# Kernel optimization log

Measured on AMD Instinct MI355X. Metric: run time of the kernel, lower is better.

Reference implementation:

```python
import jax, jax.numpy as jnp
import numpy as np

LMBDA = 100.0
GAMMA = 0.5


def _get_mask(evals1, evals2, gamma):
    # evals1, evals2: [B, K]; returns D: [B, K, K]
    scale = jnp.maximum(jnp.max(evals1, axis=1), jnp.max(evals2, axis=1))[:, None]
    e1 = evals1 / scale
    e2 = evals2 / scale
    g1 = (e1 ** gamma)[:, None, :]   # [B, 1, K]
    g2 = (e2 ** gamma)[:, :, None]   # [B, K, 1]
    M_re = g2 / (g2 ** 2 + 1) - g1 / (g1 ** 2 + 1)
    M_im = 1.0 / (g2 ** 2 + 1) - 1.0 / (g1 ** 2 + 1)
    return M_re ** 2 + M_im ** 2


def setup_inputs() -> dict:
    key = jax.random.key(0)
    ks = jax.random.split(key, 6)
    B, Vx, Vy, C, K = 8, 20000, 20000, 256, 128
    return {
        "feat_x": jax.random.normal(ks[0], (B, Vx, C), dtype=jnp.float32),
        "feat_y": jax.random.normal(ks[1], (B, Vy, C), dtype=jnp.float32),
        "evals_x": jax.random.uniform(ks[2], (B, K), dtype=jnp.float32, minval=0.01, maxval=1.0),
        "evals_y": jax.random.uniform(ks[3], (B, K), dtype=jnp.float32, minval=0.01, maxval=1.0),
        "evecs_trans_x": jax.random.normal(ks[4], (B, K, Vx), dtype=jnp.float32),
        "evecs_trans_y": jax.random.normal(ks[5], (B, K, Vy), dtype=jnp.float32),
    }


def reference(feat_x, feat_y, evals_x, evals_y, evecs_trans_x, evecs_trans_y):
    # Spectral projections of features
    A = jnp.einsum('bkv,bvc->bkc', evecs_trans_x, feat_x)   # [B, K, C]
    Bm = jnp.einsum('bkv,bvc->bkc', evecs_trans_y, feat_y)  # [B, K, C]
    D = _get_mask(evals_x, evals_y, GAMMA)                  # [B, K, K]
    AAt = jnp.einsum('bkc,bjc->bkj', A, A)                  # [B, K, K]
    BAt = jnp.einsum('bkc,bjc->bkj', Bm, A)                 # [B, K, K]
    # Batched over (B, i): solve (AAt + lmbda*diag(D[b,i])) x = BAt[b,i]
    Dmats = jax.vmap(jax.vmap(jnp.diag))(D)                 # [B, K, K, K]
    M = AAt[:, None, :, :] + LMBDA * Dmats                  # [B, K, K, K]
    Cxy = jnp.linalg.solve(M, BAt[..., None])[..., 0]       # rows: Cxy[b, i, :]
    return Cxy
```

## Files before the change

kernel.cpp:

```cpp
#include <hip/hip_runtime.h>
#include <hip/hip_bf16.h>

namespace {

constexpr int NB = 8;
constexpr int NV = 20000;
constexpr int NC = 256;
constexpr int NK = 128;
constexpr float LMBDA = 100.0f;
constexpr int KSTEP = 32;
constexpr int CHUNKS = 16;

typedef __attribute__((ext_vector_type(8))) short bf16x8;
typedef __attribute__((ext_vector_type(4))) float f32x4;

__device__ __forceinline__ uint cvtpk(float a, float c) {
  uint r;
  asm("v_cvt_pk_bf16_f32 %0, %1, %2" : "=v"(r) : "v"(a), "v"(c));
  return r;
}

template <int MODE>
__global__ __launch_bounds__(512, 4) void proj_mfma(
    const float* __restrict__ Ex, const float* __restrict__ Fx,
    const float* __restrict__ Ey, const float* __restrict__ Fy,
    float* __restrict__ A, float* __restrict__ Bm, float* __restrict__ P)
{
  extern __shared__ ushort smem[];

  const int chunk = blockIdx.x;
  const int ct    = blockIdx.y;
  const int bs    = blockIdx.z;
  const int b     = bs >> 1;
  const int side  = bs & 1;
  const float* __restrict__ E = (side ? Ey : Ex) + (size_t)b * NK * NV;
  const float* __restrict__ F = (side ? Fy : Fx) + (size_t)b * NV * NC;
  float* __restrict__ Out = (side ? Bm : A) + (size_t)b * NK * NC;
  const int cb = ct * 128;

  const int start = chunk * 39 + (chunk > 0 ? 1 : 0);
  const int nsteps = 39 + (chunk == 0 ? 1 : 0);
  const int v0 = start * KSTEP;

  const int tid  = threadIdx.x;
  const int lane = tid & 63;
  const int w    = tid >> 6;
  const int wm   = w >> 2;
  const int wn   = w & 3;
  const int lrow = lane >> 4;
  const int lcol = lane & 15;

  const int ek  = tid >> 2;
  const int evg = tid & 3;
  const int ef  = ek >> 4;
  const int entE = (((ek & 15) + evg * 4) & 15) + evg * 16;
  const float* Erow = E + (size_t)ek * NV + v0 + evg * 8;

  const int fp  = tid & 15;
  const int fc0 = (tid >> 4) * 4;
  const int fcg = fc0 >> 4;
  const int fclow = fc0 & 15;
  const int fvg = fp >> 2;
  const int fsp = fp & 3;

  f32x4 acc[4][2];
#pragma unroll
  for (int fi = 0; fi < 4; fi++)
#pragma unroll
    for (int ni = 0; ni < 2; ni++) acc[fi][ni] = (f32x4)0.f;

  const int entA = (((lcol) + lrow * 4) & 15) + lrow * 16;

  auto loadE = [&](int t, float4& a0, float4& a1) {
    const float* p = Erow + t * KSTEP;
    a0 = *(const float4*)(p);
    a1 = *(const float4*)(p + 4);
  };
  auto loadF = [&](int t, float4& b0, float4& b1) {
    const float* p = F + (size_t)(v0 + t * KSTEP + 2 * fp) * NC + cb + fc0;
    b0 = *(const float4*)(p);
    b1 = *(const float4*)(p + NC);
  };

  auto stage = [&](int buf, float4 e0, float4 e1, float4 f0, float4 f1) {
    ushort* AHb = smem + buf * 16384;
    ushort* BHb = AHb + 8192;
    const float v[8] = {e0.x, e0.y, e0.z, e0.w, e1.x, e1.y, e1.z, e1.w};
    uint hiw[4], low[4];
#pragma unroll
    for (int i = 0; i < 4; i++) {
      float a = v[2 * i], c = v[2 * i + 1];
      uint h = cvtpk(a, c);
      low[i] = cvtpk(a - __uint_as_float(h << 16),
                     c - __uint_as_float(h & 0xffff0000u));
      hiw[i] = h;
    }
    *(uint4*)(AHb + ef * 512 + entE * 8)        = make_uint4(hiw[0], hiw[1], hiw[2], hiw[3]);
    *(uint4*)(AHb + 4096 + ef * 512 + entE * 8) = make_uint4(low[0], low[1], low[2], low[3]);

    const float* fa = (const float*)&f0;
    const float* fb = (const float*)&f1;
#pragma unroll
    for (int j = 0; j < 4; j++) {
      int ent = ((fclow + j + fcg) & 15) + fvg * 16;
      float a = fa[j], c = fb[j];
      uint h = cvtpk(a, c);
      uint l = cvtpk(a - __uint_as_float(h << 16),
                     c - __uint_as_float(h & 0xffff0000u));
      *(uint*)(BHb + fcg * 512 + ent * 8 + 2 * fsp) = h;
      *(uint*)(BHb + 4096 + fcg * 512 + ent * 8 + 2 * fsp) = l;
    }
  };

  auto domfma = [&](int buf) {
    const ushort* AHb = smem + buf * 16384;
    const ushort* BHb = AHb + 8192;
    bf16x8 bHf[2], bLf[2];
#pragma unroll
    for (int ni = 0; ni < 2; ni++) {
      int cg = wn * 2 + ni;
      int entB = ((lcol + cg) & 15) + lrow * 16;
      bHf[ni] = *(const bf16x8*)(BHb + cg * 512 + entB * 8);
      bLf[ni] = *(const bf16x8*)(BHb + 4096 + cg * 512 + entB * 8);
    }
#pragma unroll
    for (int fi = 0; fi < 4; fi++) {
      bf16x8 aH = *(const bf16x8*)(AHb + (wm * 4 + fi) * 512 + entA * 8);
      bf16x8 aL = *(const bf16x8*)(AHb + 4096 + (wm * 4 + fi) * 512 + entA * 8);
#pragma unroll
      for (int ni = 0; ni < 2; ni++) {
        acc[fi][ni] = __builtin_amdgcn_mfma_f32_16x16x32_bf16(aH, bHf[ni], acc[fi][ni], 0, 0, 0);
        acc[fi][ni] = __builtin_amdgcn_mfma_f32_16x16x32_bf16(aH, bLf[ni], acc[fi][ni], 0, 0, 0);
        acc[fi][ni] = __builtin_amdgcn_mfma_f32_16x16x32_bf16(aL, bHf[ni], acc[fi][ni], 0, 0, 0);
      }
    }
  };

  float4 eA0, eA1, fA0, fA1, eB0, eB1, fB0, fB1;
  loadE(0, eA0, eA1); loadF(0, fA0, fA1);
  stage(0, eA0, eA1, fA0, fA1);
  {
    const int t1 = (1 < nsteps) ? 1 : 0;
    loadE(t1, eB0, eB1); loadF(t1, fB0, fB1);
  }
  __syncthreads();

  for (int s = 0; s < nsteps; s++) {
    const int bufc = s & 1;
    if (s + 1 < nsteps) {
      if ((s & 1) == 0) stage(bufc ^ 1, eB0, eB1, fB0, fB1);
      else              stage(bufc ^ 1, eA0, eA1, fA0, fA1);
    }
    if (s + 2 < nsteps) {
      if ((s & 1) == 0) { loadE(s + 2, eA0, eA1); loadF(s + 2, fA0, fA1); }
      else              { loadE(s + 2, eB0, eB1); loadF(s + 2, fB0, fB1); }
    }
    domfma(bufc);
    __syncthreads();
  }

#pragma unroll
  for (int fi = 0; fi < 4; fi++) {
#pragma unroll
    for (int ni = 0; ni < 2; ni++) {
      const float* av = (const float*)&acc[fi][ni];
#pragma unroll
      for (int q = 0; q < 4; q++) {
        int row = wm * 64 + fi * 16 + lrow * 4 + q;
        int col = cb + wn * 32 + ni * 16 + lcol;
        if (MODE == 0) {
          P[(((size_t)chunk * 16 + bs) * NK + row) * NC + col] = av[q];
        } else {
          atomicAdd(&Out[(size_t)row * NC + col], av[q]);
        }
      }
    }
  }
}

__global__ __launch_bounds__(256) void reduce_kernel(
    const float* __restrict__ P, float* __restrict__ AB)
{
  const int g = blockIdx.x * 256 + threadIdx.x;
  const int bsi = g >> 13;
  const int rem4 = g & 8191;
  const int side = bsi & 1, b = bsi >> 1;
  float4 s = make_float4(0.f, 0.f, 0.f, 0.f);
#pragma unroll
  for (int ch = 0; ch < CHUNKS; ch++) {
    float4 v = *(const float4*)(P + (((size_t)ch * 16 + bsi) * 8192 + rem4) * 4);
    s.x += v.x; s.y += v.y; s.z += v.z; s.w += v.w;
  }
  *(float4*)(AB + ((size_t)side * 262144 + (size_t)b * 8192 * 4 + (size_t)rem4 * 4)) = s;
}

__global__ __launch_bounds__(256) void gram_kernel(
    const float* __restrict__ A, const float* __restrict__ Bm,
    float* __restrict__ AAt, float* __restrict__ BAt)
{
  const int i0 = blockIdx.x * 8;
  const int b  = blockIdx.y;
  __shared__ float Xi[16][260];
  const float* __restrict__ Ab = A  + (size_t)b * NK * NC;
  const float* __restrict__ Bb = Bm + (size_t)b * NK * NC;
  const int tid = threadIdx.x;
  for (int idx = tid; idx < 16 * 64; idx += 256) {
    int row = idx >> 6, c4 = idx & 63;
    const float* src = (row < 8) ? (Ab + (size_t)(i0 + row) * NC)
                                 : (Bb + (size_t)(i0 + row - 8) * NC);
    *(float4*)&Xi[row][c4 * 4] = *(const float4*)(src + c4 * 4);
  }
  __syncthreads();
  const int j = tid & 127;
  const int m = tid >> 7;
  const float* __restrict__ Arow = Ab + (size_t)j * NC;
  float accv[8];
#pragma unroll
  for (int i = 0; i < 8; i++) accv[i] = 0.f;
  for (int c4 = 0; c4 < 64; c4++) {
    float4 a4 = *(const float4*)(Arow + c4 * 4);
#pragma unroll
    for (int i = 0; i < 8; i++) {
      float4 x4 = *(const float4*)&Xi[m * 8 + i][c4 * 4];
      accv[i] = fmaf(x4.x, a4.x, accv[i]);
      accv[i] = fmaf(x4.y, a4.y, accv[i]);
      accv[i] = fmaf(x4.z, a4.z, accv[i]);
      accv[i] = fmaf(x4.w, a4.w, accv[i]);
    }
  }
  float* Outp = (m ? BAt : AAt) + ((size_t)b * NK + i0) * NK + j;
#pragma unroll
  for (int i = 0; i < 8; i++) Outp[(size_t)i * NK] = accv[i];
}

__global__ __launch_bounds__(256) void mask_kernel(
    const float* __restrict__ evx, const float* __restrict__ evy,
    float* __restrict__ Dm)
{
  const int b = blockIdx.x;
  const int tid = threadIdx.x;
  __shared__ float red[256];
  __shared__ float t1x[128], t2x[128], t1y[128], t2y[128];
  float v = (tid < 128) ? evx[b * 128 + tid] : evy[b * 128 + (tid - 128)];
  red[tid] = v;
  __syncthreads();
  for (int sft = 128; sft > 0; sft >>= 1) {
    if (tid < sft) red[tid] = fmaxf(red[tid], red[tid + sft]);
    __syncthreads();
  }
  const float inv_scale = 1.0f / red[0];
  if (tid < 128) {
    float e = evx[b * 128 + tid] * inv_scale;
    float g = sqrtf(e);
    float d = 1.f / (g * g + 1.f);
    t1x[tid] = g * d;  t2x[tid] = d;
  } else {
    int i = tid - 128;
    float e = evy[b * 128 + i] * inv_scale;
    float g = sqrtf(e);
    float d = 1.f / (g * g + 1.f);
    t1y[i] = g * d;  t2y[i] = d;
  }
  __syncthreads();
  float* __restrict__ Db = Dm + (size_t)b * NK * NK;
  for (int idx = tid; idx < NK * NK; idx += 256) {
    int i = idx >> 7, jj = idx & 127;
    float re = t1y[i] - t1x[jj];
    float im = t2y[i] - t2x[jj];
    Db[idx] = re * re + im * im;
  }
}

__global__ __launch_bounds__(512) void invert_kernel(
    const float* __restrict__ AAt, float* __restrict__ Sinv)
{
  extern __shared__ float sh[];
  float* M = sh;
  float* R = sh + 128 * 132;
  const int b = blockIdx.x;
  const int tid = threadIdx.x;
  const float* __restrict__ Sb = AAt + (size_t)b * NK * NK;
  for (int idx = tid; idx < NK * NK; idx += 512) {
    M[(idx >> 7) * 132 + (idx & 127)] = Sb[idx];
  }
  __syncthreads();
  const int r = tid & 127;
  const int h = tid >> 7;
  const int c0 = h * 32;

  for (int p = 0; p < 16; p++) {
    const int J0 = p * 8;
    const bool inJ = (r >= J0) && (r < J0 + 8);
    const int i0 = r - J0;

    float g[8][8];
#pragma unroll
    for (int i = 0; i < 8; i++)
#pragma unroll
      for (int j = 0; j < 8; j++) g[i][j] = M[(J0 + i) * 132 + J0 + j];

#pragma unroll
    for (int j = 0; j < 8; j++) {
      const float invd = 1.f / g[j][j];
#pragma unroll
      for (int i = 0; i < 8; i++) {
        if (i == j) continue;
        const float f = g[i][j] * invd;
#pragma unroll
        for (int c = 0; c < 8; c++) {
          if (c == j) continue;
          g[i][c] = fmaf(-f, g[j][c], g[i][c]);
        }
        g[i][j] = -f;
      }
#pragma unroll
      for (int c = 0; c < 8; c++) {
        if (c == j) continue;
        g[j][c] *= invd;
      }
      g[j][j] = invd;
    }

    float c8[8];
    if (inJ) {
#pragma unroll
      for (int q = 0; q < 8; q++) {
        float v = 0.f;
#pragma unroll
        for (int i = 0; i < 8; i++)
          if (i0 == i) v = g[i][q];
        c8[q] = ((i0 == q) ? 1.f : 0.f) - v;
      }
    } else {
      float mr8[8];
#pragma unroll
      for (int k = 0; k < 8; k++) mr8[k] = M[r * 132 + J0 + k];
#pragma unroll
      for (int q = 0; q < 8; q++) {
        float a = 0.f;
#pragma unroll
        for (int k = 0; k < 8; k++) a = fmaf(mr8[k], g[k][q], a);
        c8[q] = a;
      }
    }

    if (inJ) {
#pragma unroll
      for (int i = 0; i < 8; i++)
        *(float4*)&R[i0 * 132 + c0 + i * 4] = *(const float4*)&M[r * 132 + c0 + i * 4];
    }
    __syncthreads();

    float4 m[8];
#pragma unroll
    for (int i = 0; i < 8; i++) m[i] = *(const float4*)&M[r * 132 + c0 + i * 4];
#pragma unroll
    for (int k = 0; k < 8; k++) {
      const float f = c8[k];
#pragma unroll
      for (int i = 0; i < 8; i++) {
        float4 rv = *(const float4*)&R[k * 132 + c0 + i * 4];
        m[i].x = fmaf(-f, rv.x, m[i].x);
        m[i].y = fmaf(-f, rv.y, m[i].y);
        m[i].z = fmaf(-f, rv.z, m[i].z);
        m[i].w = fmaf(-f, rv.w, m[i].w);
      }
    }
    {
      const bool panelH = (h == (J0 >> 5));
      const int q4 = (J0 & 31) >> 2;
      float sp[8];
#pragma unroll
      for (int q = 0; q < 8; q++)
        sp[q] = -c8[q] + ((inJ && i0 == q) ? 1.f : 0.f);
      const float4 lo = make_float4(sp[0], sp[1], sp[2], sp[3]);
      const float4 hi = make_float4(sp[4], sp[5], sp[6], sp[7]);
#pragma unroll
      for (int i = 0; i < 8; i++) {
        if (panelH && i == q4)     m[i] = lo;
        if (panelH && i == q4 + 1) m[i] = hi;
      }
    }
#pragma unroll
    for (int i = 0; i < 8; i++) *(float4*)&M[r * 132 + c0 + i * 4] = m[i];
    __syncthreads();
  }

  float* __restrict__ Ob = Sinv + (size_t)b * NK * NK;
  for (int idx = tid; idx < NK * NK; idx += 512) {
    Ob[idx] = M[(idx >> 7) * 132 + (idx & 127)];
  }
}

__global__ __launch_bounds__(256) void ns_kernel(
    const float* __restrict__ AAt, const float* __restrict__ Xin,
    float* __restrict__ Xout)
{
  extern __shared__ float sh[];
  float* S_ = sh;
  float* X_ = sh + 128 * 132;
  float* W_ = X_ + 128 * 133;
  const int tile = blockIdx.x;
  const int b    = blockIdx.y;
  const int j0   = tile * 32;
  const int tid  = threadIdx.x;
  const float* __restrict__ Sg = AAt + (size_t)b * NK * NK;
  const float* __restrict__ Xg = Xin + (size_t)b * NK * NK;
  float* __restrict__ Og       = Xout + (size_t)b * NK * NK;
  for (int idx = tid; idx < NK * NK; idx += 256) {
    int rr = idx >> 7, cc = idx & 127;
    S_[rr * 132 + cc] = Sg[idx];
    X_[rr * 133 + cc] = Xg[idx];
  }
  __syncthreads();

  const int kg  = tid >> 4;
  const int jj2 = (tid & 15) * 2;

  float aw[8][2];
#pragma unroll
  for (int u = 0; u < 8; u++) { aw[u][0] = 0.f; aw[u][1] = 0.f; }
  for (int m = 0; m < NK; m++) {
    const float x0 = X_[m * 133 + j0 + jj2];
    const float x1 = X_[m * 133 + j0 + jj2 + 1];
    float4 s0 = *(const float4*)&S_[m * 132 + kg * 8];
    float4 s1 = *(const float4*)&S_[m * 132 + kg * 8 + 4];
    const float sv[8] = {s0.x, s0.y, s0.z, s0.w, s1.x, s1.y, s1.z, s1.w};
#pragma unroll
    for (int u = 0; u < 8; u++) {
      aw[u][0] = fmaf(sv[u], x0, aw[u][0]);
      aw[u][1] = fmaf(sv[u], x1, aw[u][1]);
    }
  }
#pragma unroll
  for (int u = 0; u < 8; u++) {
#pragma unroll
    for (int j = 0; j < 2; j++) {
      const int k = kg * 8 + u;
      float val = -aw[u][j];
      if (k == j0 + jj2 + j) val += 2.f;
      W_[k * 33 + jj2 + j] = val;
    }
  }
  __syncthreads();

  float ax[8][2];
#pragma unroll
  for (int u = 0; u < 8; u++) { ax[u][0] = 0.f; ax[u][1] = 0.f; }
  for (int k = 0; k < NK; k++) {
    const float w0 = W_[k * 33 + jj2];
    const float w1 = W_[k * 33 + jj2 + 1];
#pragma unroll
    for (int u = 0; u < 8; u++) {
      const float x = X_[(kg * 8 + u) * 133 + k];
      ax[u][0] = fmaf(x, w0, ax[u][0]);
      ax[u][1] = fmaf(x, w1, ax[u][1]);
    }
  }
#pragma unroll
  for (int u = 0; u < 8; u++) {
    Og[(size_t)(kg * 8 + u) * NK + j0 + jj2]     = ax[u][0];
    Og[(size_t)(kg * 8 + u) * NK + j0 + jj2 + 1] = ax[u][1];
  }
}

__global__ __launch_bounds__(256) void solve_kernel(
    const float* __restrict__ Sinv, const float* __restrict__ BAt,
    const float* __restrict__ Dm, float* __restrict__ Cxy)
{
  extern __shared__ float sh[];
  float* SinvS = sh;
  float* ZS    = sh + 128 * 132;
  const int tile = blockIdx.x;
  const int b    = blockIdx.y;
  const int i0b  = tile * 32;
  const int tid  = threadIdx.x;
  const float* __restrict__ Sb = Sinv + (size_t)b * NK * NK;
  const float* __restrict__ Rb = BAt  + (size_t)b * NK * NK;
  const float* __restrict__ Db = Dm   + (size_t)b * NK * NK;
  for (int idx = tid; idx < NK * NK; idx += 256) {
    SinvS[(idx >> 7) * 132 + (idx & 127)] = Sb[idx];
  }
  for (int idx = tid; idx < 32 * NK; idx += 256) {
    int rr = idx >> 7, cc = idx & 127;
    ZS[rr * 133 + cc] = Rb[(size_t)(i0b + rr) * NK + cc];
  }
  __syncthreads();

  const int il = (tid >> 4) * 2;
  const int r0 = (tid & 15) * 8;
  float Y[2][8], X[2][8];
#pragma unroll
  for (int u = 0; u < 2; u++)
#pragma unroll
    for (int v = 0; v < 8; v++) Y[u][v] = 0.f;

  for (int c = 0; c < NK; c++) {
    float4 s0 = *(const float4*)&SinvS[c * 132 + r0];
    float4 s1 = *(const float4*)&SinvS[c * 132 + r0 + 4];
#pragma unroll
    for (int u = 0; u < 2; u++) {
      float z = ZS[(il + u) * 133 + c];
      Y[u][0] = fmaf(z, s0.x, Y[u][0]);
      Y[u][1] = fmaf(z, s0.y, Y[u][1]);
      Y[u][2] = fmaf(z, s0.z, Y[u][2]);
      Y[u][3] = fmaf(z, s0.w, Y[u][3]);
      Y[u][4] = fmaf(z, s1.x, Y[u][4]);
      Y[u][5] = fmaf(z, s1.y, Y[u][5]);
      Y[u][6] = fmaf(z, s1.z, Y[u][6]);
      Y[u][7] = fmaf(z, s1.w, Y[u][7]);
    }
  }
#pragma unroll
  for (int u = 0; u < 2; u++)
#pragma unroll
    for (int v = 0; v < 8; v++) X[u][v] = Y[u][v];

  for (int it = 0; it < 2; it++) {
    __syncthreads();
#pragma unroll
    for (int u = 0; u < 2; u++) {
      const float* drow = Db + (size_t)(i0b + il + u) * NK + r0;
      float* zrow = ZS + (il + u) * 133 + r0;
#pragma unroll
      for (int v = 0; v < 8; v++) zrow[v] = LMBDA * drow[v] * X[u][v];
    }
    __syncthreads();
#pragma unroll
    for (int u = 0; u < 2; u++)
#pragma unroll
      for (int v = 0; v < 8; v++) X[u][v] = Y[u][v];
    for (int c = 0; c < NK; c++) {
      float4 s0 = *(const float4*)&SinvS[c * 132 + r0];
      float4 s1 = *(const float4*)&SinvS[c * 132 + r0 + 4];
#pragma unroll
      for (int u = 0; u < 2; u++) {
        float z = ZS[(il + u) * 133 + c];
        X[u][0] = fmaf(-z, s0.x, X[u][0]);
        X[u][1] = fmaf(-z, s0.y, X[u][1]);
        X[u][2] = fmaf(-z, s0.z, X[u][2]);
        X[u][3] = fmaf(-z, s0.w, X[u][3]);
        X[u][4] = fmaf(-z, s1.x, X[u][4]);
        X[u][5] = fmaf(-z, s1.y, X[u][5]);
        X[u][6] = fmaf(-z, s1.z, X[u][6]);
        X[u][7] = fmaf(-z, s1.w, X[u][7]);
      }
    }
  }
  float* __restrict__ Ob = Cxy + ((size_t)b * NK + i0b + il) * NK + r0;
#pragma unroll
  for (int u = 0; u < 2; u++) {
    float4 o0 = make_float4(X[u][0], X[u][1], X[u][2], X[u][3]);
    float4 o1 = make_float4(X[u][4], X[u][5], X[u][6], X[u][7]);
    *(float4*)(Ob + (size_t)u * NK)     = o0;
    *(float4*)(Ob + (size_t)u * NK + 4) = o1;
  }
}

}

extern "C" void kernel_launch(void* const* d_in, const int* in_sizes, int n_in,
                              void* d_out, int out_size, void* d_ws, size_t ws_size,
                              hipStream_t stream) {
  (void)in_sizes; (void)n_in; (void)out_size;
  const float* feat_x  = (const float*)d_in[0];
  const float* feat_y  = (const float*)d_in[1];
  const float* evals_x = (const float*)d_in[2];
  const float* evals_y = (const float*)d_in[3];
  const float* etx     = (const float*)d_in[4];
  const float* ety     = (const float*)d_in[5];
  float* out = (float*)d_out;
  float* ws  = (float*)d_ws;

  float* A    = ws;
  float* Bm   = ws + 262144;
  float* AAt  = ws + 524288;
  float* BAt  = ws + 655360;
  float* Dm   = ws + 786432;
  float* Sinv = ws + 917504;
  float* P    = ws + 1048576;
  float* Sinv2 = Bm;

  const bool use_partial = ws_size >= (size_t)(1048576 + 8388608) * 4;

  constexpr int PROJ_LDS  = 2 * 16384 * 2;
  constexpr int INV_LDS   = (128 * 132 + 8 * 132) * 4;
  constexpr int NS_LDS    = (128 * 132 + 128 * 133 + 128 * 33) * 4;
  constexpr int SOLVE_LDS = (128 * 132 + 32 * 133) * 4;
  hipFuncSetAttribute((const void*)proj_mfma<0>,
                      hipFuncAttributeMaxDynamicSharedMemorySize, PROJ_LDS);
  hipFuncSetAttribute((const void*)proj_mfma<1>,
                      hipFuncAttributeMaxDynamicSharedMemorySize, PROJ_LDS);
  hipFuncSetAttribute((const void*)invert_kernel,
                      hipFuncAttributeMaxDynamicSharedMemorySize, INV_LDS);
  hipFuncSetAttribute((const void*)ns_kernel,
                      hipFuncAttributeMaxDynamicSharedMemorySize, NS_LDS);
  hipFuncSetAttribute((const void*)solve_kernel,
                      hipFuncAttributeMaxDynamicSharedMemorySize, SOLVE_LDS);

  if (use_partial) {
    proj_mfma<0><<<dim3(CHUNKS, 2, 16), 512, PROJ_LDS, stream>>>(etx, feat_x, ety, feat_y, A, Bm, P);
    reduce_kernel<<<dim3(512), 256, 0, stream>>>(P, ws);
  } else {
    hipMemsetAsync(A, 0, (size_t)524288 * sizeof(float), stream);
    proj_mfma<1><<<dim3(CHUNKS, 2, 16), 512, PROJ_LDS, stream>>>(etx, feat_x, ety, feat_y, A, Bm, P);
  }
  gram_kernel<<<dim3(16, 8), 256, 0, stream>>>(A, Bm, AAt, BAt);
  mask_kernel<<<dim3(8), 256, 0, stream>>>(evals_x, evals_y, Dm);
  invert_kernel<<<dim3(8), 512, INV_LDS, stream>>>(AAt, Sinv);
  ns_kernel<<<dim3(4, 8), 256, NS_LDS, stream>>>(AAt, Sinv, Sinv2);
  ns_kernel<<<dim3(4, 8), 256, NS_LDS, stream>>>(AAt, Sinv2, Sinv);
  solve_kernel<<<dim3(4, 8), 256, SOLVE_LDS, stream>>>(Sinv, BAt, Dm, out);
}
```

Before: 267.1 us.

## Halve projection block to 256 threads with larger per-wave MFMA tiles

Reworks the projection GEMM kernel from 512 to 256 threads per block, so each wave now computes a 64x64 output tile (4x4 MFMA fragments) instead of 64x32. The global-load and LDS staging mapping is rewritten: each thread loads 16 contiguous evec floats and eight float2 feature rows, then packs them into the hi/lo bf16 split tiles. The goal is more B-fragment reuse per LDS read and fewer threads sharing the same staging work. In exchange each thread holds more accumulators and load registers, which cuts occupancy and leaves fewer waves to hide memory latency.

```diff
diff --git a/kernel.cpp b/kernel.cpp
--- a/kernel.cpp
+++ b/kernel.cpp
@@ -21,7 +21,7 @@
 }
 
 template <int MODE>
-__global__ __launch_bounds__(512, 4) void proj_mfma(
+__global__ __launch_bounds__(256, 2) void proj_mfma(
     const float* __restrict__ Ex, const float* __restrict__ Fx,
     const float* __restrict__ Ey, const float* __restrict__ Fy,
     float* __restrict__ A, float* __restrict__ Bm, float* __restrict__ P)
@@ -45,80 +45,99 @@
   const int tid  = threadIdx.x;
   const int lane = tid & 63;
   const int w    = tid >> 6;
-  const int wm   = w >> 2;
-  const int wn   = w & 3;
+  const int wm   = w >> 1;
+  const int wn   = w & 1;
   const int lrow = lane >> 4;
   const int lcol = lane & 15;
 
-  const int ek  = tid >> 2;
-  const int evg = tid & 3;
-  const int ef  = ek >> 4;
-  const int entE = (((ek & 15) + evg * 4) & 15) + evg * 16;
-  const float* Erow = E + (size_t)ek * NV + v0 + evg * 8;
-
-  const int fp  = tid & 15;
-  const int fc0 = (tid >> 4) * 4;
-  const int fcg = fc0 >> 4;
-  const int fclow = fc0 & 15;
-  const int fvg = fp >> 2;
-  const int fsp = fp & 3;
-
-  f32x4 acc[4][2];
+  const int erow = tid >> 1;
+  const int eh   = tid & 1;
+  const float* Erow = E + (size_t)erow * NV + v0 + eh * 16;
+
+  const int bg  = tid >> 6;
+  const int c0  = (tid & 63) * 2;
+  const int c1  = c0 + 1;
+  const float* Fbase = F + (size_t)(v0 + bg * 8) * NC + cb + c0;
+
+  f32x4 acc[4][4];
 #pragma unroll
   for (int fi = 0; fi < 4; fi++)
 #pragma unroll
-    for (int ni = 0; ni < 2; ni++) acc[fi][ni] = (f32x4)0.f;
+    for (int ni = 0; ni < 4; ni++) acc[fi][ni] = (f32x4)0.f;
 
   const int entA = (((lcol) + lrow * 4) & 15) + lrow * 16;
 
-  auto loadE = [&](int t, float4& a0, float4& a1) {
+  auto loadE = [&](int t, float4* e) {
     const float* p = Erow + t * KSTEP;
-    a0 = *(const float4*)(p);
-    a1 = *(const float4*)(p + 4);
+    e[0] = *(const float4*)(p);
+    e[1] = *(const float4*)(p + 4);
+    e[2] = *(const float4*)(p + 8);
+    e[3] = *(const float4*)(p + 12);
   };
-  auto loadF = [&](int t, float4& b0, float4& b1) {
-    const float* p = F + (size_t)(v0 + t * KSTEP + 2 * fp) * NC + cb + fc0;
-    b0 = *(const float4*)(p);
-    b1 = *(const float4*)(p + NC);
+  auto loadF = [&](int t, float2* f) {
+    const float* p = Fbase + (size_t)t * KSTEP * NC;
+#pragma unroll
+    for (int j = 0; j < 8; j++) f[j] = *(const float2*)(p + (size_t)j * NC);
   };
 
-  auto stage = [&](int buf, float4 e0, float4 e1, float4 f0, float4 f1) {
+  auto stage = [&](int buf, const float4* e, const float2* f) {
     ushort* AHb = smem + buf * 16384;
     ushort* BHb = AHb + 8192;
-    const float v[8] = {e0.x, e0.y, e0.z, e0.w, e1.x, e1.y, e1.z, e1.w};
-    uint hiw[4], low[4];
-#pragma unroll
-    for (int i = 0; i < 4; i++) {
-      float a = v[2 * i], c = v[2 * i + 1];
-      uint h = cvtpk(a, c);
-      low[i] = cvtpk(a - __uint_as_float(h << 16),
-                     c - __uint_as_float(h & 0xffff0000u));
-      hiw[i] = h;
-    }
-    *(uint4*)(AHb + ef * 512 + entE * 8)        = make_uint4(hiw[0], hiw[1], hiw[2], hiw[3]);
-    *(uint4*)(AHb + 4096 + ef * 512 + entE * 8) = make_uint4(low[0], low[1], low[2], low[3]);
-
-    const float* fa = (const float*)&f0;
-    const float* fb = (const float*)&f1;
-#pragma unroll
-    for (int j = 0; j < 4; j++) {
-      int ent = ((fclow + j + fcg) & 15) + fvg * 16;
-      float a = fa[j], c = fb[j];
-      uint h = cvtpk(a, c);
-      uint l = cvtpk(a - __uint_as_float(h << 16),
-                     c - __uint_as_float(h & 0xffff0000u));
-      *(uint*)(BHb + fcg * 512 + ent * 8 + 2 * fsp) = h;
-      *(uint*)(BHb + 4096 + fcg * 512 + ent * 8 + 2 * fsp) = l;
+    {
+      const int frag = erow >> 4;
+      const int r15  = erow & 15;
+#pragma unroll
+      for (int i = 0; i < 2; i++) {
+        const int vg  = 2 * eh + i;
+        const int ent = ((r15 + vg * 4) & 15) + vg * 16;
+        const float4 x = e[2 * i];
+        const float4 y = e[2 * i + 1];
+        uint h0 = cvtpk(x.x, x.y), h1 = cvtpk(x.z, x.w);
+        uint h2 = cvtpk(y.x, y.y), h3 = cvtpk(y.z, y.w);
+        uint l0 = cvtpk(x.x - __uint_as_float(h0 << 16),
+                        x.y - __uint_as_float(h0 & 0xffff0000u));
+        uint l1 = cvtpk(x.z - __uint_as_float(h1 << 16),
+                        x.w - __uint_as_float(h1 & 0xffff0000u));
+        uint l2 = cvtpk(y.x - __uint_as_float(h2 << 16),
+                        y.y - __uint_as_float(h2 & 0xffff0000u));
+        uint l3 = cvtpk(y.z - __uint_as_float(h3 << 16),
+                        y.w - __uint_as_float(h3 & 0xffff0000u));
+        *(uint4*)(AHb + frag * 512 + ent * 8)        = make_uint4(h0, h1, h2, h3);
+        *(uint4*)(AHb + 4096 + frag * 512 + ent * 8) = make_uint4(l0, l1, l2, l3);
+      }
+    }
+    {
+      const int frag = c0 >> 4;
+      const int ent0 = (((c0 & 15) + frag) & 15) + bg * 16;
+      const int ent1 = (((c1 & 15) + frag) & 15) + bg * 16;
+      uint h0[4], l0[4], h1[4], l1[4];
+#pragma unroll
+      for (int i = 0; i < 4; i++) {
+        const float a0 = f[2 * i].x, b0 = f[2 * i + 1].x;
+        const float a1 = f[2 * i].y, b1 = f[2 * i + 1].y;
+        uint h = cvtpk(a0, b0);
+        h0[i] = h;
+        l0[i] = cvtpk(a0 - __uint_as_float(h << 16),
+                      b0 - __uint_as_float(h & 0xffff0000u));
+        h = cvtpk(a1, b1);
+        h1[i] = h;
+        l1[i] = cvtpk(a1 - __uint_as_float(h << 16),
+                      b1 - __uint_as_float(h & 0xffff0000u));
+      }
+      *(uint4*)(BHb + frag * 512 + ent0 * 8)        = make_uint4(h0[0], h0[1], h0[2], h0[3]);
+      *(uint4*)(BHb + 4096 + frag * 512 + ent0 * 8) = make_uint4(l0[0], l0[1], l0[2], l0[3]);
+      *(uint4*)(BHb + frag * 512 + ent1 * 8)        = make_uint4(h1[0], h1[1], h1[2], h1[3]);
+      *(uint4*)(BHb + 4096 + frag * 512 + ent1 * 8) = make_uint4(l1[0], l1[1], l1[2], l1[3]);
     }
   };
 
   auto domfma = [&](int buf) {
     const ushort* AHb = smem + buf * 16384;
     const ushort* BHb = AHb + 8192;
-    bf16x8 bHf[2], bLf[2];
-#pragma unroll
-    for (int ni = 0; ni < 2; ni++) {
-      int cg = wn * 2 + ni;
+    bf16x8 bHf[4], bLf[4];
+#pragma unroll
+    for (int ni = 0; ni < 4; ni++) {
+      int cg = wn * 4 + ni;
       int entB = ((lcol + cg) & 15) + lrow * 16;
       bHf[ni] = *(const bf16x8*)(BHb + cg * 512 + entB * 8);
       bLf[ni] = *(const bf16x8*)(BHb + 4096 + cg * 512 + entB * 8);
@@ -128,7 +147,7 @@
       bf16x8 aH = *(const bf16x8*)(AHb + (wm * 4 + fi) * 512 + entA * 8);
       bf16x8 aL = *(const bf16x8*)(AHb + 4096 + (wm * 4 + fi) * 512 + entA * 8);
 #pragma unroll
-      for (int ni = 0; ni < 2; ni++) {
+      for (int ni = 0; ni < 4; ni++) {
         acc[fi][ni] = __builtin_amdgcn_mfma_f32_16x16x32_bf16(aH, bHf[ni], acc[fi][ni], 0, 0, 0);
         acc[fi][ni] = __builtin_amdgcn_mfma_f32_16x16x32_bf16(aH, bLf[ni], acc[fi][ni], 0, 0, 0);
         acc[fi][ni] = __builtin_amdgcn_mfma_f32_16x16x32_bf16(aL, bHf[ni], acc[fi][ni], 0, 0, 0);
@@ -136,24 +155,25 @@
     }
   };
 
-  float4 eA0, eA1, fA0, fA1, eB0, eB1, fB0, fB1;
-  loadE(0, eA0, eA1); loadF(0, fA0, fA1);
-  stage(0, eA0, eA1, fA0, fA1);
+  float4 eA[4]; float2 fA[8];
+  float4 eB[4]; float2 fB[8];
+  loadE(0, eA); loadF(0, fA);
+  stage(0, eA, fA);
   {
     const int t1 = (1 < nsteps) ? 1 : 0;
-    loadE(t1, eB0, eB1); loadF(t1, fB0, fB1);
+    loadE(t1, eB); loadF(t1, fB);
   }
   __syncthreads();
 
   for (int s = 0; s < nsteps; s++) {
     const int bufc = s & 1;
     if (s + 1 < nsteps) {
-      if ((s & 1) == 0) stage(bufc ^ 1, eB0, eB1, fB0, fB1);
-      else              stage(bufc ^ 1, eA0, eA1, fA0, fA1);
+      if ((s & 1) == 0) stage(bufc ^ 1, eB, fB);
+      else              stage(bufc ^ 1, eA, fA);
     }
     if (s + 2 < nsteps) {
-      if ((s & 1) == 0) { loadE(s + 2, eA0, eA1); loadF(s + 2, fA0, fA1); }
-      else              { loadE(s + 2, eB0, eB1); loadF(s + 2, fB0, fB1); }
+      if ((s & 1) == 0) { loadE(s + 2, eA); loadF(s + 2, fA); }
+      else              { loadE(s + 2, eB); loadF(s + 2, fB); }
     }
     domfma(bufc);
     __syncthreads();
@@ -162,12 +182,12 @@
 #pragma unroll
   for (int fi = 0; fi < 4; fi++) {
 #pragma unroll
-    for (int ni = 0; ni < 2; ni++) {
+    for (int ni = 0; ni < 4; ni++) {
       const float* av = (const float*)&acc[fi][ni];
 #pragma unroll
       for (int q = 0; q < 4; q++) {
         int row = wm * 64 + fi * 16 + lrow * 4 + q;
-        int col = cb + wn * 32 + ni * 16 + lcol;
+        int col = cb + wn * 64 + ni * 16 + lcol;
         if (MODE == 0) {
           P[(((size_t)chunk * 16 + bs) * NK + row) * NC + col] = av[q];
         } else {
@@ -599,11 +619,11 @@
                       hipFuncAttributeMaxDynamicSharedMemorySize, SOLVE_LDS);
 
   if (use_partial) {
-    proj_mfma<0><<<dim3(CHUNKS, 2, 16), 512, PROJ_LDS, stream>>>(etx, feat_x, ety, feat_y, A, Bm, P);
+    proj_mfma<0><<<dim3(CHUNKS, 2, 16), 256, PROJ_LDS, stream>>>(etx, feat_x, ety, feat_y, A, Bm, P);
     reduce_kernel<<<dim3(512), 256, 0, stream>>>(P, ws);
   } else {
     hipMemsetAsync(A, 0, (size_t)524288 * sizeof(float), stream);
-    proj_mfma<1><<<dim3(CHUNKS, 2, 16), 512, PROJ_LDS, stream>>>(etx, feat_x, ety, feat_y, A, Bm, P);
+    proj_mfma<1><<<dim3(CHUNKS, 2, 16), 256, PROJ_LDS, stream>>>(etx, feat_x, ety, feat_y, A, Bm, P);
   }
   gram_kernel<<<dim3(16, 8), 256, 0, stream>>>(A, Bm, AAt, BAt);
   mask_kernel<<<dim3(8), 256, 0, stream>>>(evals_x, evals_y, Dm);
```

Measured after the change: 272.3 us. About the same (+2.0%).

## Double chunk count, single-buffer static LDS, atomically fold chunk pairs

Applied to the files above, without the earlier changes.

Splits the vertex dimension into 32 chunks instead of 16, so twice as many blocks run the projection GEMM, each over roughly half as many steps. The double-buffered dynamic LDS pipeline is replaced with a single static buffer and two barriers per step, with only the next global load prefetched into registers. Pairs of chunks now accumulate into the existing 16 partial slots with atomicAdd, which needs a memset of the partial buffer first. The goal is more parallelism and occupancy, at the cost of less latency hiding, an extra memset pass and atomic traffic.

```diff
diff --git a/kernel.cpp b/kernel.cpp
--- a/kernel.cpp
+++ b/kernel.cpp
@@ -9,7 +9,7 @@
 constexpr int NK = 128;
 constexpr float LMBDA = 100.0f;
 constexpr int KSTEP = 32;
-constexpr int CHUNKS = 16;
+constexpr int CHUNKS = 32;
 
 typedef __attribute__((ext_vector_type(8))) short bf16x8;
 typedef __attribute__((ext_vector_type(4))) float f32x4;
@@ -21,13 +21,11 @@
 }
 
 template <int MODE>
-__global__ __launch_bounds__(512, 4) void proj_mfma(
+__global__ __launch_bounds__(512) void proj_mfma(
     const float* __restrict__ Ex, const float* __restrict__ Fx,
     const float* __restrict__ Ey, const float* __restrict__ Fy,
     float* __restrict__ A, float* __restrict__ Bm, float* __restrict__ P)
 {
-  extern __shared__ ushort smem[];
-
   const int chunk = blockIdx.x;
   const int ct    = blockIdx.y;
   const int bs    = blockIdx.z;
@@ -38,9 +36,12 @@
   float* __restrict__ Out = (side ? Bm : A) + (size_t)b * NK * NC;
   const int cb = ct * 128;
 
-  const int start = chunk * 39 + (chunk > 0 ? 1 : 0);
-  const int nsteps = 39 + (chunk == 0 ? 1 : 0);
+  const int nsteps = (chunk < 17) ? 20 : 19;
+  const int start  = (chunk < 17) ? 20 * chunk : 340 + 19 * (chunk - 17);
   const int v0 = start * KSTEP;
+
+  __shared__ __align__(16) ushort AH[2][8][64][8];
+  __shared__ __align__(16) ushort BH[2][8][64][8];
 
   const int tid  = threadIdx.x;
   const int lane = tid & 63;
@@ -82,9 +83,7 @@
     b1 = *(const float4*)(p + NC);
   };
 
-  auto stage = [&](int buf, float4 e0, float4 e1, float4 f0, float4 f1) {
-    ushort* AHb = smem + buf * 16384;
-    ushort* BHb = AHb + 8192;
+  auto stage = [&](float4 e0, float4 e1, float4 f0, float4 f1) {
     const float v[8] = {e0.x, e0.y, e0.z, e0.w, e1.x, e1.y, e1.z, e1.w};
     uint hiw[4], low[4];
 #pragma unroll
@@ -95,8 +94,8 @@
                      c - __uint_as_float(h & 0xffff0000u));
       hiw[i] = h;
     }
-    *(uint4*)(AHb + ef * 512 + entE * 8)        = make_uint4(hiw[0], hiw[1], hiw[2], hiw[3]);
-    *(uint4*)(AHb + 4096 + ef * 512 + entE * 8) = make_uint4(low[0], low[1], low[2], low[3]);
+    *(uint4*)&AH[0][ef][entE][0] = make_uint4(hiw[0], hiw[1], hiw[2], hiw[3]);
+    *(uint4*)&AH[1][ef][entE][0] = make_uint4(low[0], low[1], low[2], low[3]);
 
     const float* fa = (const float*)&f0;
     const float* fb = (const float*)&f1;
@@ -107,26 +106,24 @@
       uint h = cvtpk(a, c);
       uint l = cvtpk(a - __uint_as_float(h << 16),
                      c - __uint_as_float(h & 0xffff0000u));
-      *(uint*)(BHb + fcg * 512 + ent * 8 + 2 * fsp) = h;
-      *(uint*)(BHb + 4096 + fcg * 512 + ent * 8 + 2 * fsp) = l;
+      *(uint*)&BH[0][fcg][ent][2 * fsp] = h;
+      *(uint*)&BH[1][fcg][ent][2 * fsp] = l;
     }
   };
 
-  auto domfma = [&](int buf) {
-    const ushort* AHb = smem + buf * 16384;
-    const ushort* BHb = AHb + 8192;
+  auto domfma = [&]() {
     bf16x8 bHf[2], bLf[2];
 #pragma unroll
     for (int ni = 0; ni < 2; ni++) {
       int cg = wn * 2 + ni;
       int entB = ((lcol + cg) & 15) + lrow * 16;
-      bHf[ni] = *(const bf16x8*)(BHb + cg * 512 + entB * 8);
-      bLf[ni] = *(const bf16x8*)(BHb + 4096 + cg * 512 + entB * 8);
+      bHf[ni] = *(const bf16x8*)&BH[0][cg][entB][0];
+      bLf[ni] = *(const bf16x8*)&BH[1][cg][entB][0];
     }
 #pragma unroll
     for (int fi = 0; fi < 4; fi++) {
-      bf16x8 aH = *(const bf16x8*)(AHb + (wm * 4 + fi) * 512 + entA * 8);
-      bf16x8 aL = *(const bf16x8*)(AHb + 4096 + (wm * 4 + fi) * 512 + entA * 8);
+      bf16x8 aH = *(const bf16x8*)&AH[0][wm * 4 + fi][entA][0];
+      bf16x8 aL = *(const bf16x8*)&AH[1][wm * 4 + fi][entA][0];
 #pragma unroll
       for (int ni = 0; ni < 2; ni++) {
         acc[fi][ni] = __builtin_amdgcn_mfma_f32_16x16x32_bf16(aH, bHf[ni], acc[fi][ni], 0, 0, 0);
@@ -136,26 +133,13 @@
     }
   };
 
-  float4 eA0, eA1, fA0, fA1, eB0, eB1, fB0, fB1;
-  loadE(0, eA0, eA1); loadF(0, fA0, fA1);
-  stage(0, eA0, eA1, fA0, fA1);
-  {
-    const int t1 = (1 < nsteps) ? 1 : 0;
-    loadE(t1, eB0, eB1); loadF(t1, fB0, fB1);
-  }
-  __syncthreads();
-
+  float4 e0, e1, f0, f1;
+  loadE(0, e0, e1); loadF(0, f0, f1);
   for (int s = 0; s < nsteps; s++) {
-    const int bufc = s & 1;
-    if (s + 1 < nsteps) {
-      if ((s & 1) == 0) stage(bufc ^ 1, eB0, eB1, fB0, fB1);
-      else              stage(bufc ^ 1, eA0, eA1, fA0, fA1);
-    }
-    if (s + 2 < nsteps) {
-      if ((s & 1) == 0) { loadE(s + 2, eA0, eA1); loadF(s + 2, fA0, fA1); }
-      else              { loadE(s + 2, eB0, eB1); loadF(s + 2, fB0, fB1); }
-    }
-    domfma(bufc);
+    stage(e0, e1, f0, f1);
+    __syncthreads();
+    if (s + 1 < nsteps) { loadE(s + 1, e0, e1); loadF(s + 1, f0, f1); }
+    domfma();
     __syncthreads();
   }
 
@@ -169,7 +153,7 @@
         int row = wm * 64 + fi * 16 + lrow * 4 + q;
         int col = cb + wn * 32 + ni * 16 + lcol;
         if (MODE == 0) {
-          P[(((size_t)chunk * 16 + bs) * NK + row) * NC + col] = av[q];
+          atomicAdd(&P[(((size_t)(chunk >> 1) * 16 + bs) * NK + row) * NC + col], av[q]);
         } else {
           atomicAdd(&Out[(size_t)row * NC + col], av[q]);
         }
@@ -187,7 +171,7 @@
   const int side = bsi & 1, b = bsi >> 1;
   float4 s = make_float4(0.f, 0.f, 0.f, 0.f);
 #pragma unroll
-  for (int ch = 0; ch < CHUNKS; ch++) {
+  for (int ch = 0; ch < 16; ch++) {
     float4 v = *(const float4*)(P + (((size_t)ch * 16 + bsi) * 8192 + rem4) * 4);
     s.x += v.x; s.y += v.y; s.z += v.z; s.w += v.w;
   }
@@ -583,14 +567,9 @@
 
   const bool use_partial = ws_size >= (size_t)(1048576 + 8388608) * 4;
 
-  constexpr int PROJ_LDS  = 2 * 16384 * 2;
   constexpr int INV_LDS   = (128 * 132 + 8 * 132) * 4;
   constexpr int NS_LDS    = (128 * 132 + 128 * 133 + 128 * 33) * 4;
   constexpr int SOLVE_LDS = (128 * 132 + 32 * 133) * 4;
-  hipFuncSetAttribute((const void*)proj_mfma<0>,
-                      hipFuncAttributeMaxDynamicSharedMemorySize, PROJ_LDS);
-  hipFuncSetAttribute((const void*)proj_mfma<1>,
-                      hipFuncAttributeMaxDynamicSharedMemorySize, PROJ_LDS);
   hipFuncSetAttribute((const void*)invert_kernel,
                       hipFuncAttributeMaxDynamicSharedMemorySize, INV_LDS);
   hipFuncSetAttribute((const void*)ns_kernel,
@@ -599,11 +578,12 @@
                       hipFuncAttributeMaxDynamicSharedMemorySize, SOLVE_LDS);
 
   if (use_partial) {
-    proj_mfma<0><<<dim3(CHUNKS, 2, 16), 512, PROJ_LDS, stream>>>(etx, feat_x, ety, feat_y, A, Bm, P);
+    hipMemsetAsync(P, 0, (size_t)8388608 * sizeof(float), stream);
+    proj_mfma<0><<<dim3(CHUNKS, 2, 16), 512, 0, stream>>>(etx, feat_x, ety, feat_y, A, Bm, P);
     reduce_kernel<<<dim3(512), 256, 0, stream>>>(P, ws);
   } else {
     hipMemsetAsync(A, 0, (size_t)524288 * sizeof(float), stream);
-    proj_mfma<1><<<dim3(CHUNKS, 2, 16), 512, PROJ_LDS, stream>>>(etx, feat_x, ety, feat_y, A, Bm, P);
+    proj_mfma<1><<<dim3(CHUNKS, 2, 16), 512, 0, stream>>>(etx, feat_x, ety, feat_y, A, Bm, P);
   }
   gram_kernel<<<dim3(16, 8), 256, 0, stream>>>(A, Bm, AAt, BAt);
   mask_kernel<<<dim3(8), 256, 0, stream>>>(evals_x, evals_y, Dm);
```

Measured after the change: 302.0 us. +13.0%, slower.

## Stream E tiles into LDS via direct global_load_lds and split at MFMA time

Applied to the files above, without the earlier changes.

Loads of the eigenvector (E) operand now go straight from global memory into LDS as raw fp32 using the direct global-to-LDS load instruction, with an XOR swizzle. Each wave converts its rows to bf16 hi/lo pairs when it reads them for the MFMA, instead of staging converted values through registers. This removes register staging and the pre-conversion pass for E, and lets the E load overlap across the double buffer. The cost is that fp32 tiles double the LDS footprint for E. Conversion work is also repeated per wave, since each wn wave converts the same rows, and the fenceless DMA relies on the existing barriers.

```diff
diff --git a/kernel.cpp b/kernel.cpp
--- a/kernel.cpp
+++ b/kernel.cpp
@@ -14,6 +14,9 @@
 typedef __attribute__((ext_vector_type(8))) short bf16x8;
 typedef __attribute__((ext_vector_type(4))) float f32x4;
 
+typedef const __attribute__((address_space(1))) uint gl_uint;
+typedef __attribute__((address_space(3))) uint lds_uint;
+
 __device__ __forceinline__ uint cvtpk(float a, float c) {
   uint r;
   asm("v_cvt_pk_bf16_f32 %0, %1, %2" : "=v"(r) : "v"(a), "v"(c));
@@ -26,7 +29,9 @@
     const float* __restrict__ Ey, const float* __restrict__ Fy,
     float* __restrict__ A, float* __restrict__ Bm, float* __restrict__ P)
 {
-  extern __shared__ ushort smem[];
+  extern __shared__ __align__(16) ushort smem[];
+  float*  Epool = (float*)smem;
+  ushort* Bpool = smem + 16384;
 
   const int chunk = blockIdx.x;
   const int ct    = blockIdx.y;
@@ -50,12 +55,6 @@
   const int lrow = lane >> 4;
   const int lcol = lane & 15;
 
-  const int ek  = tid >> 2;
-  const int evg = tid & 3;
-  const int ef  = ek >> 4;
-  const int entE = (((ek & 15) + evg * 4) & 15) + evg * 16;
-  const float* Erow = E + (size_t)ek * NV + v0 + evg * 8;
-
   const int fp  = tid & 15;
   const int fc0 = (tid >> 4) * 4;
   const int fcg = fc0 >> 4;
@@ -69,35 +68,27 @@
 #pragma unroll
     for (int ni = 0; ni < 2; ni++) acc[fi][ni] = (f32x4)0.f;
 
-  const int entA = (((lcol) + lrow * 4) & 15) + lrow * 16;
-
-  auto loadE = [&](int t, float4& a0, float4& a1) {
-    const float* p = Erow + t * KSTEP;
-    a0 = *(const float4*)(p);
-    a1 = *(const float4*)(p + 4);
+  auto dmaE = [&](int t, int buf) {
+    float* Eb = Epool + buf * 4096;
+#pragma unroll
+    for (int c = 0; c < 2; c++) {
+      const int r   = c * 64 + (tid >> 3);
+      const int v4p = tid & 7;
+      const int v4  = v4p ^ (r & 7);
+      const float* src = E + (size_t)r * NV + v0 + t * KSTEP + v4 * 4;
+      float* dst = Eb + c * 2048 + w * 256;
+      __builtin_amdgcn_global_load_lds((gl_uint*)src, (lds_uint*)dst, 16, 0, 0);
+    }
   };
+
   auto loadF = [&](int t, float4& b0, float4& b1) {
     const float* p = F + (size_t)(v0 + t * KSTEP + 2 * fp) * NC + cb + fc0;
     b0 = *(const float4*)(p);
     b1 = *(const float4*)(p + NC);
   };
 
-  auto stage = [&](int buf, float4 e0, float4 e1, float4 f0, float4 f1) {
-    ushort* AHb = smem + buf * 16384;
-    ushort* BHb = AHb + 8192;
-    const float v[8] = {e0.x, e0.y, e0.z, e0.w, e1.x, e1.y, e1.z, e1.w};
-    uint hiw[4], low[4];
-#pragma unroll
-    for (int i = 0; i < 4; i++) {
-      float a = v[2 * i], c = v[2 * i + 1];
-      uint h = cvtpk(a, c);
-      low[i] = cvtpk(a - __uint_as_float(h << 16),
-                     c - __uint_as_float(h & 0xffff0000u));
-      hiw[i] = h;
-    }
-    *(uint4*)(AHb + ef * 512 + entE * 8)        = make_uint4(hiw[0], hiw[1], hiw[2], hiw[3]);
-    *(uint4*)(AHb + 4096 + ef * 512 + entE * 8) = make_uint4(low[0], low[1], low[2], low[3]);
-
+  auto stageB = [&](int buf, float4 f0, float4 f1) {
+    ushort* BHb = Bpool + buf * 8192;
     const float* fa = (const float*)&f0;
     const float* fb = (const float*)&f1;
 #pragma unroll
@@ -113,8 +104,8 @@
   };
 
   auto domfma = [&](int buf) {
-    const ushort* AHb = smem + buf * 16384;
-    const ushort* BHb = AHb + 8192;
+    const float*  Eb  = Epool + buf * 4096;
+    const ushort* BHb = Bpool + buf * 8192;
     bf16x8 bHf[2], bLf[2];
 #pragma unroll
     for (int ni = 0; ni < 2; ni++) {
@@ -125,8 +116,24 @@
     }
 #pragma unroll
     for (int fi = 0; fi < 4; fi++) {
-      bf16x8 aH = *(const bf16x8*)(AHb + (wm * 4 + fi) * 512 + entA * 8);
-      bf16x8 aL = *(const bf16x8*)(AHb + 4096 + (wm * 4 + fi) * 512 + entA * 8);
+      const int row = wm * 64 + fi * 16 + lcol;
+      const int sw  = row & 7;
+      const float4 x = *(const float4*)(Eb + row * 32 + ((lrow * 2 + 0) ^ sw) * 4);
+      const float4 y = *(const float4*)(Eb + row * 32 + ((lrow * 2 + 1) ^ sw) * 4);
+      const uint h0 = cvtpk(x.x, x.y), h1 = cvtpk(x.z, x.w);
+      const uint h2 = cvtpk(y.x, y.y), h3 = cvtpk(y.z, y.w);
+      const uint l0 = cvtpk(x.x - __uint_as_float(h0 << 16),
+                            x.y - __uint_as_float(h0 & 0xffff0000u));
+      const uint l1 = cvtpk(x.z - __uint_as_float(h1 << 16),
+                            x.w - __uint_as_float(h1 & 0xffff0000u));
+      const uint l2 = cvtpk(y.x - __uint_as_float(h2 << 16),
+                            y.y - __uint_as_float(h2 & 0xffff0000u));
+      const uint l3 = cvtpk(y.z - __uint_as_float(h3 << 16),
+                            y.w - __uint_as_float(h3 & 0xffff0000u));
+      const uint4 ahv = make_uint4(h0, h1, h2, h3);
+      const uint4 alv = make_uint4(l0, l1, l2, l3);
+      bf16x8 aH = *(const bf16x8*)&ahv;
+      bf16x8 aL = *(const bf16x8*)&alv;
 #pragma unroll
       for (int ni = 0; ni < 2; ni++) {
         acc[fi][ni] = __builtin_amdgcn_mfma_f32_16x16x32_bf16(aH, bHf[ni], acc[fi][ni], 0, 0, 0);
@@ -136,24 +143,23 @@
     }
   };
 
-  float4 eA0, eA1, fA0, fA1, eB0, eB1, fB0, fB1;
-  loadE(0, eA0, eA1); loadF(0, fA0, fA1);
-  stage(0, eA0, eA1, fA0, fA1);
-  {
-    const int t1 = (1 < nsteps) ? 1 : 0;
-    loadE(t1, eB0, eB1); loadF(t1, fB0, fB1);
-  }
+  float4 fA0, fA1, fB0, fB1;
+  dmaE(0, 0);
+  loadF(0, fA0, fA1);
+  stageB(0, fA0, fA1);
+  if (1 < nsteps) loadF(1, fB0, fB1);
   __syncthreads();
 
   for (int s = 0; s < nsteps; s++) {
     const int bufc = s & 1;
     if (s + 1 < nsteps) {
-      if ((s & 1) == 0) stage(bufc ^ 1, eB0, eB1, fB0, fB1);
-      else              stage(bufc ^ 1, eA0, eA1, fA0, fA1);
+      dmaE(s + 1, bufc ^ 1);
+      if ((s & 1) == 0) stageB(bufc ^ 1, fB0, fB1);
+      else              stageB(bufc ^ 1, fA0, fA1);
     }
     if (s + 2 < nsteps) {
-      if ((s & 1) == 0) { loadE(s + 2, eA0, eA1); loadF(s + 2, fA0, fA1); }
-      else              { loadE(s + 2, eB0, eB1); loadF(s + 2, fB0, fB1); }
+      if ((s & 1) == 0) loadF(s + 2, fA0, fA1);
+      else              loadF(s + 2, fB0, fB1);
     }
     domfma(bufc);
     __syncthreads();
@@ -583,7 +589,7 @@
 
   const bool use_partial = ws_size >= (size_t)(1048576 + 8388608) * 4;
 
-  constexpr int PROJ_LDS  = 2 * 16384 * 2;
+  constexpr int PROJ_LDS  = 65536;
   constexpr int INV_LDS   = (128 * 132 + 8 * 132) * 4;
   constexpr int NS_LDS    = (128 * 132 + 128 * 133 + 128 * 33) * 4;
   constexpr int SOLVE_LDS = (128 * 132 + 32 * 133) * 4;
```

Measured after the change: 270.4 us. About the same (+1.2%).
